# Optimization experiments

Measured on AMD Instinct MI355X. Metric: run time of the kernel, lower is better.

## Reference

```python
import jax, jax.numpy as jnp
import numpy as np

N = 50000
E = 600000
D_IN, D_HID, D_OUT = 128, 128, 64


def gcn_conv(x, edge_index, W, b):
    """PyG GCNConv: add self-loops, symmetric deg^{-1/2} normalization,
    linear transform, scatter-add aggregation, bias."""
    n = x.shape[0]
    loop = jnp.arange(n, dtype=edge_index.dtype)
    src = jnp.concatenate([edge_index[0], loop])
    dst = jnp.concatenate([edge_index[1], loop])
    h = x @ W  # [N, out]
    deg = jax.ops.segment_sum(jnp.ones_like(dst, dtype=h.dtype), dst, num_segments=n)
    dinv = jnp.where(deg > 0, jax.lax.rsqrt(jnp.maximum(deg, 1e-12)), 0.0)
    norm = dinv[src] * dinv[dst]  # [E+N]
    msg = h[src] * norm[:, None]  # gather + scale
    out = jax.ops.segment_sum(msg, dst, num_segments=n)  # scatter-add
    return out + b


def setup_inputs() -> dict:
    key = jax.random.key(0)
    k1, k2, k3, k4 = jax.random.split(key, 4)
    x = jax.random.normal(k1, (N, D_IN), dtype=jnp.float32)
    edge_index = jax.random.randint(k2, (2, E), 0, N, dtype=jnp.int64)
    s1 = (1.0 / np.sqrt(D_IN)).astype(np.float32) if False else np.float32(1.0 / np.sqrt(D_IN))
    s2 = np.float32(1.0 / np.sqrt(D_HID))
    W1 = jax.random.normal(k3, (D_IN, D_HID), dtype=jnp.float32) * s1
    b1 = jnp.zeros((D_HID,), dtype=jnp.float32)
    W2 = jax.random.normal(k4, (D_HID, D_OUT), dtype=jnp.float32) * s2
    b2 = jnp.zeros((D_OUT,), dtype=jnp.float32)
    return {"x": x, "edge_index": edge_index, "W1": W1, "b1": b1, "W2": W2, "b2": b2}


def reference(x, edge_index, W1, b1, W2, b2):
    # eval mode: dropout p = 0
    h = jax.nn.relu(gcn_conv(x, edge_index, W1, b1))
    return gcn_conv(h, edge_index, W2, b2)
```

## Files before the change

kernel.cpp:

```cpp
#include <hip/hip_runtime.h>
#include <hip/hip_bf16.h>
#include <stdint.h>

#define DIN 128
#define DHID 128
#define DOUT2 64

__device__ __forceinline__ unsigned short f2bf(float f) {
    unsigned u = __float_as_uint(f);
    u += 0x7fffu + ((u >> 16) & 1u);
    return (unsigned short)(u >> 16);
}
__device__ __forceinline__ float bf2f(unsigned short b) {
    return __uint_as_float(((unsigned)b) << 16);
}
__device__ __forceinline__ float bflo(unsigned v) { return __uint_as_float(v << 16); }
__device__ __forceinline__ float bfhi(unsigned v) { return __uint_as_float(v & 0xffff0000u); }

__global__ void detect_i64_kernel(const unsigned* ei, int* flag) {
    int t = threadIdx.x;
    unsigned hi = ei[2 * t + 1];
    unsigned long long vote = __ballot(hi == 0u);
    if (t == 0) *flag = (vote == ~0ull) ? 1 : 0;
}

__global__ void deg_count_kernel(const int* ei32, const long long* ei64, const int* flag,
                                 unsigned* deg, int E) {
    int e = blockIdx.x * blockDim.x + threadIdx.x;
    if (e >= E) return;
    int mode = *flag;
    int d = mode ? (int)ei64[(size_t)E + e] : ei32[(size_t)E + e];
    atomicAdd(&deg[d], 1u);
}

__global__ void dinv_kernel(const unsigned* deg, float* dinv, int N) {
    int i = blockIdx.x * blockDim.x + threadIdx.x;
    if (i < N) dinv[i] = 1.0f / sqrtf((float)(deg[i] + 1u));
}

__global__ __launch_bounds__(256) void scan_blocksum_kernel(const unsigned* deg, int* bsum,
                                                            int N) {
    __shared__ int s[256];
    int t = threadIdx.x;
    int base = blockIdx.x * 1024 + t * 4;
    int sum = 0;
    if (base + 3 < N) {
        int4 v = *(const int4*)((const int*)deg + base);
        sum = v.x + v.y + v.z + v.w;
    } else {
        for (int j = 0; j < 4; j++)
            if (base + j < N) sum += (int)deg[base + j];
    }
    s[t] = sum;
    __syncthreads();
    for (int off = 128; off > 0; off >>= 1) {
        if (t < off) s[t] += s[t + off];
        __syncthreads();
    }
    if (t == 0) bsum[blockIdx.x] = s[0];
}

__global__ __launch_bounds__(256) void scan_bsum_kernel(int* bsum, int* row_ptr, int nb, int N) {
    __shared__ int s[256];
    int t = threadIdx.x;
    int v = (t < nb) ? bsum[t] : 0;
    s[t] = v;
    __syncthreads();
    for (int off = 1; off < 256; off <<= 1) {
        int u = (t >= off) ? s[t - off] : 0;
        __syncthreads();
        s[t] += u;
        __syncthreads();
    }
    if (t < nb) bsum[t] = s[t] - v;
    if (t == 255) row_ptr[N] = s[255];
}

__global__ __launch_bounds__(256) void scan_write_kernel(const unsigned* deg, const int* bsum,
                                                         int* row_ptr, int* cursor, int N) {
    __shared__ int s[256];
    int t = threadIdx.x;
    int base = blockIdx.x * 1024 + t * 4;
    int d[4];
    int sum = 0;
#pragma unroll
    for (int j = 0; j < 4; j++) {
        int idx = base + j;
        d[j] = (idx < N) ? (int)deg[idx] : 0;
        sum += d[j];
    }
    s[t] = sum;
    __syncthreads();
    for (int off = 1; off < 256; off <<= 1) {
        int u = (t >= off) ? s[t - off] : 0;
        __syncthreads();
        s[t] += u;
        __syncthreads();
    }
    int run = bsum[blockIdx.x] + s[t] - sum;
#pragma unroll
    for (int j = 0; j < 4; j++) {
        int idx = base + j;
        if (idx < N) {
            row_ptr[idx] = run;
            cursor[idx] = run;
            run += d[j];
        }
    }
}

__global__ void scatter_kernel(const int* ei32, const long long* ei64, const int* flag,
                               const float* dinv, int* cursor, int* csr_src, float* csr_w,
                               int E) {
    int e = blockIdx.x * blockDim.x + threadIdx.x;
    if (e >= E) return;
    int mode = *flag;
    int s, d;
    if (mode) {
        s = (int)ei64[e];
        d = (int)ei64[(size_t)E + e];
    } else {
        s = ei32[e];
        d = ei32[(size_t)E + e];
    }
    int pos = atomicAdd(&cursor[d], 1);
    csr_src[pos] = s;
    csr_w[pos] = dinv[s];
}

template <int DO, typename AT>
__global__ __launch_bounds__(256, 2) void gemm_kernel(const AT* __restrict__ A,
                                                      const float* __restrict__ W,
                                                      unsigned short* __restrict__ out, int M) {
    constexpr int CG  = DO / 4;
    constexpr int TYN = 256 / CG;
    constexpr int RM  = 64 / TYN;
    __shared__ float As[64 * 64];
    __shared__ float Bs[64 * DO];
    const int tid = threadIdx.x;
    const int row0 = blockIdx.x * 64;
    const int tx = tid % CG, ty = tid / CG;

    float acc[RM][4];
#pragma unroll
    for (int r = 0; r < RM; r++) acc[r][0] = acc[r][1] = acc[r][2] = acc[r][3] = 0.f;

    for (int k0 = 0; k0 < 128; k0 += 64) {
        for (int idx = tid; idx < 64 * 16; idx += 256) {
            int r = idx >> 4, cc = idx & 15;
            int row = row0 + r;
            float4 v = make_float4(0.f, 0.f, 0.f, 0.f);
            if (row < M) {
                if constexpr (sizeof(AT) == 4) {
                    v = ((const float4*)A)[(size_t)row * 32 + (k0 >> 2) + cc];
                } else {
                    ushort4 u = ((const ushort4*)A)[(size_t)row * 32 + (k0 >> 2) + cc];
                    v = make_float4(bf2f(u.x), bf2f(u.y), bf2f(u.z), bf2f(u.w));
                }
            }
            ((float4*)As)[idx] = v;
        }
        for (int idx = tid; idx < 64 * CG; idx += 256) {
            int r = idx / CG, cc = idx % CG;
            ((float4*)Bs)[idx] = ((const float4*)W)[(size_t)(k0 + r) * CG + cc];
        }
        __syncthreads();
#pragma unroll 8
        for (int k = 0; k < 64; k++) {
            float4 b = ((const float4*)Bs)[k * CG + tx];
#pragma unroll
            for (int r = 0; r < RM; r++) {
                float a = As[(ty * RM + r) * 64 + k];
                acc[r][0] = fmaf(a, b.x, acc[r][0]);
                acc[r][1] = fmaf(a, b.y, acc[r][1]);
                acc[r][2] = fmaf(a, b.z, acc[r][2]);
                acc[r][3] = fmaf(a, b.w, acc[r][3]);
            }
        }
        __syncthreads();
    }
#pragma unroll
    for (int r = 0; r < RM; r++) {
        int row = row0 + ty * RM + r;
        if (row < M) {
            ushort4 v;
            v.x = f2bf(acc[r][0]);
            v.y = f2bf(acc[r][1]);
            v.z = f2bf(acc[r][2]);
            v.w = f2bf(acc[r][3]);
            ((ushort4*)out)[(size_t)row * CG + tx] = v;
        }
    }
}

template <int D, bool RELU, typename OT>
__global__ __launch_bounds__(256) void agg_kernel(const unsigned short* __restrict__ h,
                                                  const int* __restrict__ csr_src,
                                                  const float* __restrict__ csr_w,
                                                  const int* __restrict__ row_ptr,
                                                  const float* __restrict__ dinv,
                                                  const float* __restrict__ bias,
                                                  OT* __restrict__ out, int N) {
    const int wid = threadIdx.x >> 6;
    const int lane = threadIdx.x & 63;
    const int i = blockIdx.x * 4 + wid;
    if (i >= N) return;
    const float di = dinv[i];
    const int start = row_ptr[i], end = row_ptr[i + 1];

    if constexpr (D == 128) {
        const unsigned* hu = (const unsigned*)h;
        unsigned sv = hu[(size_t)i * 64 + lane];
        float a0 = di * bflo(sv), b0 = di * bfhi(sv);
        float a1 = 0.f, b1 = 0.f;
        int j = start;
        for (; j + 4 <= end; j += 4) {
            int s0 = csr_src[j], s1 = csr_src[j + 1], s2 = csr_src[j + 2], s3 = csr_src[j + 3];
            float w0 = csr_w[j], w1 = csr_w[j + 1], w2 = csr_w[j + 2], w3 = csr_w[j + 3];
            unsigned v0 = hu[(size_t)s0 * 64 + lane];
            unsigned v1 = hu[(size_t)s1 * 64 + lane];
            unsigned v2 = hu[(size_t)s2 * 64 + lane];
            unsigned v3 = hu[(size_t)s3 * 64 + lane];
            a0 = fmaf(w0, bflo(v0), a0);
            b0 = fmaf(w0, bfhi(v0), b0);
            a1 = fmaf(w1, bflo(v1), a1);
            b1 = fmaf(w1, bfhi(v1), b1);
            a0 = fmaf(w2, bflo(v2), a0);
            b0 = fmaf(w2, bfhi(v2), b0);
            a1 = fmaf(w3, bflo(v3), a1);
            b1 = fmaf(w3, bfhi(v3), b1);
        }
        for (; j < end; ++j) {
            int s0 = csr_src[j];
            float w0 = csr_w[j];
            unsigned v0 = hu[(size_t)s0 * 64 + lane];
            a0 = fmaf(w0, bflo(v0), a0);
            b0 = fmaf(w0, bfhi(v0), b0);
        }
        float rx = di * (a0 + a1) + bias[2 * lane];
        float ry = di * (b0 + b1) + bias[2 * lane + 1];
        if (RELU) {
            rx = fmaxf(rx, 0.f);
            ry = fmaxf(ry, 0.f);
        }
        if constexpr (sizeof(OT) == 2) {
            unsigned pv = (unsigned)f2bf(rx) | ((unsigned)f2bf(ry) << 16);
            ((unsigned*)out)[(size_t)i * 64 + lane] = pv;
        } else {
            float2 pv = make_float2(rx, ry);
            ((float2*)out)[(size_t)i * 64 + lane] = pv;
        }
    } else {
        float a0 = di * bf2f(h[(size_t)i * 64 + lane]);
        float a1 = 0.f;
        int j = start;
        for (; j + 4 <= end; j += 4) {
            int s0 = csr_src[j], s1 = csr_src[j + 1], s2 = csr_src[j + 2], s3 = csr_src[j + 3];
            float w0 = csr_w[j], w1 = csr_w[j + 1], w2 = csr_w[j + 2], w3 = csr_w[j + 3];
            float v0 = bf2f(h[(size_t)s0 * 64 + lane]);
            float v1 = bf2f(h[(size_t)s1 * 64 + lane]);
            float v2 = bf2f(h[(size_t)s2 * 64 + lane]);
            float v3 = bf2f(h[(size_t)s3 * 64 + lane]);
            a0 = fmaf(w0, v0, a0);
            a1 = fmaf(w1, v1, a1);
            a0 = fmaf(w2, v2, a0);
            a1 = fmaf(w3, v3, a1);
        }
        for (; j < end; ++j) {
            a0 = fmaf(csr_w[j], bf2f(h[(size_t)csr_src[j] * 64 + lane]), a0);
        }
        float r = di * (a0 + a1) + bias[lane];
        if (RELU) r = fmaxf(r, 0.f);
        if constexpr (sizeof(OT) == 2) {
            out[(size_t)i * 64 + lane] = (OT)f2bf(r);
        } else {
            out[(size_t)i * 64 + lane] = r;
        }
    }
}

extern "C" void kernel_launch(void* const* d_in, const int* in_sizes, int n_in,
                              void* d_out, int out_size, void* d_ws, size_t ws_size,
                              hipStream_t stream) {
    const float* x  = (const float*)d_in[0];
    const void*  ei = d_in[1];
    const float* W1 = (const float*)d_in[2];
    const float* b1 = (const float*)d_in[3];
    const float* W2 = (const float*)d_in[4];
    const float* b2 = (const float*)d_in[5];
    float* out = (float*)d_out;

    const int N = in_sizes[0] / DIN;
    const int E = in_sizes[1] / 2;

    char* ws = (char*)d_ws;
    size_t off = 0;
    auto alloc = [&](size_t bytes) -> void* {
        void* p = ws + off;
        off += (bytes + 255) & ~(size_t)255;
        return p;
    };
    unsigned*       deg  = (unsigned*)alloc((size_t)N * 4);
    float*          dinv = (float*)alloc((size_t)N * 4);
    int*            rowp = (int*)alloc((size_t)(N + 1) * 4);
    int*            curs = (int*)alloc((size_t)N * 4);
    int*            flag = (int*)alloc(256);
    int*            bsum = (int*)alloc(1024 * 4);
    int*            csrs = (int*)alloc((size_t)E * 4);
    float*          csrw = (float*)alloc((size_t)E * 4);
    unsigned short* h1   = (unsigned short*)alloc((size_t)N * DHID * 2);
    unsigned short* o1   = (unsigned short*)alloc((size_t)N * DHID * 2);
    unsigned short* h2   = h1;

    const int nb = (N + 1023) / 1024;

    hipMemsetAsync(deg, 0, (size_t)N * 4, stream);
    detect_i64_kernel<<<1, 64, 0, stream>>>((const unsigned*)ei, flag);
    deg_count_kernel<<<(E + 255) / 256, 256, 0, stream>>>((const int*)ei, (const long long*)ei,
                                                          flag, deg, E);
    dinv_kernel<<<(N + 255) / 256, 256, 0, stream>>>(deg, dinv, N);
    scan_blocksum_kernel<<<nb, 256, 0, stream>>>(deg, bsum, N);
    scan_bsum_kernel<<<1, 256, 0, stream>>>(bsum, rowp, nb, N);
    scan_write_kernel<<<nb, 256, 0, stream>>>(deg, bsum, rowp, curs, N);
    scatter_kernel<<<(E + 255) / 256, 256, 0, stream>>>((const int*)ei, (const long long*)ei,
                                                        flag, dinv, curs, csrs, csrw, E);
    gemm_kernel<DHID, float><<<(N + 63) / 64, 256, 0, stream>>>(x, W1, h1, N);
    agg_kernel<DHID, true, unsigned short><<<(N + 3) / 4, 256, 0, stream>>>(h1, csrs, csrw, rowp,
                                                                            dinv, b1, o1, N);
    gemm_kernel<DOUT2, unsigned short><<<(N + 63) / 64, 256, 0, stream>>>(o1, W2, h2, N);
    agg_kernel<DOUT2, false, float><<<(N + 3) / 4, 256, 0, stream>>>(h2, csrs, csrw, rowp, dinv,
                                                                     b2, out, N);
}
```

Baseline: 274.6 us.

## Fuse degree count with first GEMM, fold dinv into scan, pack CSR entries

Runs the layer-1 GEMM and the degree-count atomics in one launch so the independent work can overlap, and computes dinv inside the block-sum scan kernel, which removes two launches. When N fits in 16 bits, each CSR entry is packed into a single 32-bit word holding the source index and an fp16 copy of its dinv weight. This halves CSR traffic in both aggregation passes. The cost is fp16 rounding of the edge weights and a second code path for large graphs.

```diff
diff --git a/kernel.cpp b/kernel.cpp
--- a/kernel.cpp
+++ b/kernel.cpp
@@ -1,5 +1,5 @@
 #include <hip/hip_runtime.h>
-#include <hip/hip_bf16.h>
+#include <hip/hip_fp16.h>
 #include <stdint.h>
 
 #define DIN 128
@@ -16,6 +16,12 @@
 }
 __device__ __forceinline__ float bflo(unsigned v) { return __uint_as_float(v << 16); }
 __device__ __forceinline__ float bfhi(unsigned v) { return __uint_as_float(v & 0xffff0000u); }
+__device__ __forceinline__ unsigned short f2h(float f) {
+    return __half_as_ushort(__float2half_rn(f));
+}
+__device__ __forceinline__ float h2f(unsigned bits) {
+    return __half2float(__ushort_as_half((unsigned short)bits));
+}
 
 __global__ void detect_i64_kernel(const unsigned* ei, int* flag) {
     int t = threadIdx.x;
@@ -24,121 +30,15 @@
     if (t == 0) *flag = (vote == ~0ull) ? 1 : 0;
 }
 
-__global__ void deg_count_kernel(const int* ei32, const long long* ei64, const int* flag,
-                                 unsigned* deg, int E) {
-    int e = blockIdx.x * blockDim.x + threadIdx.x;
-    if (e >= E) return;
-    int mode = *flag;
-    int d = mode ? (int)ei64[(size_t)E + e] : ei32[(size_t)E + e];
-    atomicAdd(&deg[d], 1u);
-}
-
-__global__ void dinv_kernel(const unsigned* deg, float* dinv, int N) {
-    int i = blockIdx.x * blockDim.x + threadIdx.x;
-    if (i < N) dinv[i] = 1.0f / sqrtf((float)(deg[i] + 1u));
-}
-
-__global__ __launch_bounds__(256) void scan_blocksum_kernel(const unsigned* deg, int* bsum,
-                                                            int N) {
-    __shared__ int s[256];
-    int t = threadIdx.x;
-    int base = blockIdx.x * 1024 + t * 4;
-    int sum = 0;
-    if (base + 3 < N) {
-        int4 v = *(const int4*)((const int*)deg + base);
-        sum = v.x + v.y + v.z + v.w;
-    } else {
-        for (int j = 0; j < 4; j++)
-            if (base + j < N) sum += (int)deg[base + j];
-    }
-    s[t] = sum;
-    __syncthreads();
-    for (int off = 128; off > 0; off >>= 1) {
-        if (t < off) s[t] += s[t + off];
-        __syncthreads();
-    }
-    if (t == 0) bsum[blockIdx.x] = s[0];
-}
-
-__global__ __launch_bounds__(256) void scan_bsum_kernel(int* bsum, int* row_ptr, int nb, int N) {
-    __shared__ int s[256];
-    int t = threadIdx.x;
-    int v = (t < nb) ? bsum[t] : 0;
-    s[t] = v;
-    __syncthreads();
-    for (int off = 1; off < 256; off <<= 1) {
-        int u = (t >= off) ? s[t - off] : 0;
-        __syncthreads();
-        s[t] += u;
-        __syncthreads();
-    }
-    if (t < nb) bsum[t] = s[t] - v;
-    if (t == 255) row_ptr[N] = s[255];
-}
-
-__global__ __launch_bounds__(256) void scan_write_kernel(const unsigned* deg, const int* bsum,
-                                                         int* row_ptr, int* cursor, int N) {
-    __shared__ int s[256];
-    int t = threadIdx.x;
-    int base = blockIdx.x * 1024 + t * 4;
-    int d[4];
-    int sum = 0;
-#pragma unroll
-    for (int j = 0; j < 4; j++) {
-        int idx = base + j;
-        d[j] = (idx < N) ? (int)deg[idx] : 0;
-        sum += d[j];
-    }
-    s[t] = sum;
-    __syncthreads();
-    for (int off = 1; off < 256; off <<= 1) {
-        int u = (t >= off) ? s[t - off] : 0;
-        __syncthreads();
-        s[t] += u;
-        __syncthreads();
-    }
-    int run = bsum[blockIdx.x] + s[t] - sum;
-#pragma unroll
-    for (int j = 0; j < 4; j++) {
-        int idx = base + j;
-        if (idx < N) {
-            row_ptr[idx] = run;
-            cursor[idx] = run;
-            run += d[j];
-        }
-    }
-}
-
-__global__ void scatter_kernel(const int* ei32, const long long* ei64, const int* flag,
-                               const float* dinv, int* cursor, int* csr_src, float* csr_w,
-                               int E) {
-    int e = blockIdx.x * blockDim.x + threadIdx.x;
-    if (e >= E) return;
-    int mode = *flag;
-    int s, d;
-    if (mode) {
-        s = (int)ei64[e];
-        d = (int)ei64[(size_t)E + e];
-    } else {
-        s = ei32[e];
-        d = ei32[(size_t)E + e];
-    }
-    int pos = atomicAdd(&cursor[d], 1);
-    csr_src[pos] = s;
-    csr_w[pos] = dinv[s];
-}
-
 template <int DO, typename AT>
-__global__ __launch_bounds__(256, 2) void gemm_kernel(const AT* __restrict__ A,
-                                                      const float* __restrict__ W,
-                                                      unsigned short* __restrict__ out, int M) {
+__device__ __forceinline__ void gemm_block(const AT* __restrict__ A, const float* __restrict__ W,
+                                           unsigned short* __restrict__ out, int M, int bx,
+                                           float* As, float* Bs) {
     constexpr int CG  = DO / 4;
     constexpr int TYN = 256 / CG;
     constexpr int RM  = 64 / TYN;
-    __shared__ float As[64 * 64];
-    __shared__ float Bs[64 * DO];
     const int tid = threadIdx.x;
-    const int row0 = blockIdx.x * 64;
+    const int row0 = bx * 64;
     const int tx = tid % CG, ty = tid / CG;
 
     float acc[RM][4];
@@ -193,10 +93,162 @@
     }
 }
 
-template <int D, bool RELU, typename OT>
+__global__ __launch_bounds__(256, 2) void fused_gemm_deg_kernel(
+    const float* __restrict__ A, const float* __restrict__ W, unsigned short* __restrict__ out,
+    int M, int gemmBlocks, const int* ei32, const long long* ei64, const int* flag,
+    unsigned* deg, int E) {
+    __shared__ float As[64 * 64];
+    __shared__ float Bs[64 * DHID];
+    if ((int)blockIdx.x < gemmBlocks) {
+        gemm_block<DHID, float>(A, W, out, M, blockIdx.x, As, Bs);
+    } else {
+        int e = (blockIdx.x - gemmBlocks) * 256 + threadIdx.x;
+        if (e < E) {
+            int mode = *flag;
+            int d = mode ? (int)ei64[(size_t)E + e] : ei32[(size_t)E + e];
+            atomicAdd(&deg[d], 1u);
+        }
+    }
+}
+
+template <int DO, typename AT>
+__global__ __launch_bounds__(256, 2) void gemm_kernel(const AT* __restrict__ A,
+                                                      const float* __restrict__ W,
+                                                      unsigned short* __restrict__ out, int M) {
+    __shared__ float As[64 * 64];
+    __shared__ float Bs[64 * DO];
+    gemm_block<DO, AT>(A, W, out, M, blockIdx.x, As, Bs);
+}
+
+__global__ __launch_bounds__(256) void scan_blocksum_kernel(const unsigned* deg, int* bsum,
+                                                            float* dinv, int N) {
+    __shared__ int s[256];
+    int t = threadIdx.x;
+    int base = blockIdx.x * 1024 + t * 4;
+    int sum = 0;
+    if (base + 3 < N) {
+        int4 v = *(const int4*)((const int*)deg + base);
+        sum = v.x + v.y + v.z + v.w;
+        float4 dv;
+        dv.x = rsqrtf((float)(v.x + 1));
+        dv.y = rsqrtf((float)(v.y + 1));
+        dv.z = rsqrtf((float)(v.z + 1));
+        dv.w = rsqrtf((float)(v.w + 1));
+        *(float4*)(dinv + base) = dv;
+    } else {
+        for (int j = 0; j < 4; j++)
+            if (base + j < N) {
+                int d = (int)deg[base + j];
+                sum += d;
+                dinv[base + j] = rsqrtf((float)(d + 1));
+            }
+    }
+    s[t] = sum;
+    __syncthreads();
+    for (int off = 128; off > 0; off >>= 1) {
+        if (t < off) s[t] += s[t + off];
+        __syncthreads();
+    }
+    if (t == 0) bsum[blockIdx.x] = s[0];
+}
+
+__global__ __launch_bounds__(256) void scan_bsum_kernel(int* bsum, int* row_ptr, int nb, int N) {
+    __shared__ int s[256];
+    int t = threadIdx.x;
+    int v = (t < nb) ? bsum[t] : 0;
+    s[t] = v;
+    __syncthreads();
+    for (int off = 1; off < 256; off <<= 1) {
+        int u = (t >= off) ? s[t - off] : 0;
+        __syncthreads();
+        s[t] += u;
+        __syncthreads();
+    }
+    if (t < nb) bsum[t] = s[t] - v;
+    if (t == 255) row_ptr[N] = s[255];
+}
+
+__global__ __launch_bounds__(256) void scan_write_kernel(const unsigned* deg, const int* bsum,
+                                                         int* row_ptr, int* cursor, int N) {
+    __shared__ int s[256];
+    int t = threadIdx.x;
+    int base = blockIdx.x * 1024 + t * 4;
+    int d[4];
+    int sum = 0;
+#pragma unroll
+    for (int j = 0; j < 4; j++) {
+        int idx = base + j;
+        d[j] = (idx < N) ? (int)deg[idx] : 0;
+        sum += d[j];
+    }
+    s[t] = sum;
+    __syncthreads();
+    for (int off = 1; off < 256; off <<= 1) {
+        int u = (t >= off) ? s[t - off] : 0;
+        __syncthreads();
+        s[t] += u;
+        __syncthreads();
+    }
+    int run = bsum[blockIdx.x] + s[t] - sum;
+#pragma unroll
+    for (int j = 0; j < 4; j++) {
+        int idx = base + j;
+        if (idx < N) {
+            row_ptr[idx] = run;
+            cursor[idx] = run;
+            run += d[j];
+        }
+    }
+}
+
+__global__ void scatter_pack32_kernel(const int* ei32, const long long* ei64, const int* flag,
+                                      const float* dinv, int* cursor, unsigned* csr, int E) {
+    int e = blockIdx.x * blockDim.x + threadIdx.x;
+    if (e >= E) return;
+    int mode = *flag;
+    int s, d;
+    if (mode) {
+        s = (int)ei64[e];
+        d = (int)ei64[(size_t)E + e];
+    } else {
+        s = ei32[e];
+        d = ei32[(size_t)E + e];
+    }
+    int pos = atomicAdd(&cursor[d], 1);
+    csr[pos] = (unsigned)s | ((unsigned)f2h(dinv[s]) << 16);
+}
+
+__global__ void scatter_pack64_kernel(const int* ei32, const long long* ei64, const int* flag,
+                                      const float* dinv, int* cursor, unsigned long long* csr,
+                                      int E) {
+    int e = blockIdx.x * blockDim.x + threadIdx.x;
+    if (e >= E) return;
+    int mode = *flag;
+    int s, d;
+    if (mode) {
+        s = (int)ei64[e];
+        d = (int)ei64[(size_t)E + e];
+    } else {
+        s = ei32[e];
+        d = ei32[(size_t)E + e];
+    }
+    int pos = atomicAdd(&cursor[d], 1);
+    csr[pos] = (unsigned long long)(unsigned)s |
+               ((unsigned long long)__float_as_uint(dinv[s]) << 32);
+}
+
+__device__ __forceinline__ void unpack(unsigned p, int& s, float& w) {
+    s = (int)(p & 0xffffu);
+    w = h2f(p >> 16);
+}
+__device__ __forceinline__ void unpack(unsigned long long p, int& s, float& w) {
+    s = (int)(unsigned)(p & 0xffffffffu);
+    w = __uint_as_float((unsigned)(p >> 32));
+}
+
+template <int D, bool RELU, typename OT, typename CT>
 __global__ __launch_bounds__(256) void agg_kernel(const unsigned short* __restrict__ h,
-                                                  const int* __restrict__ csr_src,
-                                                  const float* __restrict__ csr_w,
+                                                  const CT* __restrict__ csr,
                                                   const int* __restrict__ row_ptr,
                                                   const float* __restrict__ dinv,
                                                   const float* __restrict__ bias,
@@ -215,8 +267,13 @@
         float a1 = 0.f, b1 = 0.f;
         int j = start;
         for (; j + 4 <= end; j += 4) {
-            int s0 = csr_src[j], s1 = csr_src[j + 1], s2 = csr_src[j + 2], s3 = csr_src[j + 3];
-            float w0 = csr_w[j], w1 = csr_w[j + 1], w2 = csr_w[j + 2], w3 = csr_w[j + 3];
+            CT p0 = csr[j], p1 = csr[j + 1], p2 = csr[j + 2], p3 = csr[j + 3];
+            int s0, s1, s2, s3;
+            float w0, w1, w2, w3;
+            unpack(p0, s0, w0);
+            unpack(p1, s1, w1);
+            unpack(p2, s2, w2);
+            unpack(p3, s3, w3);
             unsigned v0 = hu[(size_t)s0 * 64 + lane];
             unsigned v1 = hu[(size_t)s1 * 64 + lane];
             unsigned v2 = hu[(size_t)s2 * 64 + lane];
@@ -231,14 +288,16 @@
             b1 = fmaf(w3, bfhi(v3), b1);
         }
         for (; j < end; ++j) {
-            int s0 = csr_src[j];
-            float w0 = csr_w[j];
+            int s0;
+            float w0;
+            unpack(csr[j], s0, w0);
             unsigned v0 = hu[(size_t)s0 * 64 + lane];
             a0 = fmaf(w0, bflo(v0), a0);
             b0 = fmaf(w0, bfhi(v0), b0);
         }
-        float rx = di * (a0 + a1) + bias[2 * lane];
-        float ry = di * (b0 + b1) + bias[2 * lane + 1];
+        float2 bv = ((const float2*)bias)[lane];
+        float rx = di * (a0 + a1) + bv.x;
+        float ry = di * (b0 + b1) + bv.y;
         if (RELU) {
             rx = fmaxf(rx, 0.f);
             ry = fmaxf(ry, 0.f);
@@ -247,16 +306,20 @@
             unsigned pv = (unsigned)f2bf(rx) | ((unsigned)f2bf(ry) << 16);
             ((unsigned*)out)[(size_t)i * 64 + lane] = pv;
         } else {
-            float2 pv = make_float2(rx, ry);
-            ((float2*)out)[(size_t)i * 64 + lane] = pv;
+            ((float2*)out)[(size_t)i * 64 + lane] = make_float2(rx, ry);
         }
     } else {
         float a0 = di * bf2f(h[(size_t)i * 64 + lane]);
         float a1 = 0.f;
         int j = start;
         for (; j + 4 <= end; j += 4) {
-            int s0 = csr_src[j], s1 = csr_src[j + 1], s2 = csr_src[j + 2], s3 = csr_src[j + 3];
-            float w0 = csr_w[j], w1 = csr_w[j + 1], w2 = csr_w[j + 2], w3 = csr_w[j + 3];
+            CT p0 = csr[j], p1 = csr[j + 1], p2 = csr[j + 2], p3 = csr[j + 3];
+            int s0, s1, s2, s3;
+            float w0, w1, w2, w3;
+            unpack(p0, s0, w0);
+            unpack(p1, s1, w1);
+            unpack(p2, s2, w2);
+            unpack(p3, s3, w3);
             float v0 = bf2f(h[(size_t)s0 * 64 + lane]);
             float v1 = bf2f(h[(size_t)s1 * 64 + lane]);
             float v2 = bf2f(h[(size_t)s2 * 64 + lane]);
@@ -267,7 +330,10 @@
             a1 = fmaf(w3, v3, a1);
         }
         for (; j < end; ++j) {
-            a0 = fmaf(csr_w[j], bf2f(h[(size_t)csr_src[j] * 64 + lane]), a0);
+            int s0;
+            float w0;
+            unpack(csr[j], s0, w0);
+            a0 = fmaf(w0, bf2f(h[(size_t)s0 * 64 + lane]), a0);
         }
         float r = di * (a0 + a1) + bias[lane];
         if (RELU) r = fmaxf(r, 0.f);
@@ -306,28 +372,41 @@
     int*            curs = (int*)alloc((size_t)N * 4);
     int*            flag = (int*)alloc(256);
     int*            bsum = (int*)alloc(1024 * 4);
-    int*            csrs = (int*)alloc((size_t)E * 4);
-    float*          csrw = (float*)alloc((size_t)E * 4);
+    void*           csr  = alloc((size_t)E * 8);
     unsigned short* h1   = (unsigned short*)alloc((size_t)N * DHID * 2);
     unsigned short* o1   = (unsigned short*)alloc((size_t)N * DHID * 2);
     unsigned short* h2   = h1;
 
     const int nb = (N + 1023) / 1024;
+    const int gemmBlocks = (N + 63) / 64;
+    const int degBlocks = (E + 255) / 256;
 
     hipMemsetAsync(deg, 0, (size_t)N * 4, stream);
     detect_i64_kernel<<<1, 64, 0, stream>>>((const unsigned*)ei, flag);
-    deg_count_kernel<<<(E + 255) / 256, 256, 0, stream>>>((const int*)ei, (const long long*)ei,
-                                                          flag, deg, E);
-    dinv_kernel<<<(N + 255) / 256, 256, 0, stream>>>(deg, dinv, N);
-    scan_blocksum_kernel<<<nb, 256, 0, stream>>>(deg, bsum, N);
+    fused_gemm_deg_kernel<<<gemmBlocks + degBlocks, 256, 0, stream>>>(
+        x, W1, h1, N, gemmBlocks, (const int*)ei, (const long long*)ei, flag, deg, E);
+    scan_blocksum_kernel<<<nb, 256, 0, stream>>>(deg, bsum, dinv, N);
     scan_bsum_kernel<<<1, 256, 0, stream>>>(bsum, rowp, nb, N);
     scan_write_kernel<<<nb, 256, 0, stream>>>(deg, bsum, rowp, curs, N);
-    scatter_kernel<<<(E + 255) / 256, 256, 0, stream>>>((const int*)ei, (const long long*)ei,
-                                                        flag, dinv, curs, csrs, csrw, E);
-    gemm_kernel<DHID, float><<<(N + 63) / 64, 256, 0, stream>>>(x, W1, h1, N);
-    agg_kernel<DHID, true, unsigned short><<<(N + 3) / 4, 256, 0, stream>>>(h1, csrs, csrw, rowp,
-                                                                            dinv, b1, o1, N);
-    gemm_kernel<DOUT2, unsigned short><<<(N + 63) / 64, 256, 0, stream>>>(o1, W2, h2, N);
-    agg_kernel<DOUT2, false, float><<<(N + 3) / 4, 256, 0, stream>>>(h2, csrs, csrw, rowp, dinv,
-                                                                     b2, out, N);
-}
+
+    if (N <= 65535) {
+        unsigned* csr32 = (unsigned*)csr;
+        scatter_pack32_kernel<<<degBlocks, 256, 0, stream>>>(
+            (const int*)ei, (const long long*)ei, flag, dinv, curs, csr32, E);
+        agg_kernel<DHID, true, unsigned short, unsigned><<<(N + 3) / 4, 256, 0, stream>>>(
+            h1, csr32, rowp, dinv, b1, o1, N);
+        gemm_kernel<DOUT2, unsigned short><<<gemmBlocks, 256, 0, stream>>>(o1, W2, h2, N);
+        agg_kernel<DOUT2, false, float, unsigned><<<(N + 3) / 4, 256, 0, stream>>>(
+            h2, csr32, rowp, dinv, b2, out, N);
+    } else {
+        unsigned long long* csr64 = (unsigned long long*)csr;
+        scatter_pack64_kernel<<<degBlocks, 256, 0, stream>>>(
+            (const int*)ei, (const long long*)ei, flag, dinv, curs, csr64, E);
+        agg_kernel<DHID, true, unsigned short, unsigned long long><<<(N + 3) / 4, 256, 0,
+                                                                     stream>>>(h1, csr64, rowp,
+                                                                               dinv, b1, o1, N);
+        gemm_kernel<DOUT2, unsigned short><<<gemmBlocks, 256, 0, stream>>>(o1, W2, h2, N);
+        agg_kernel<DOUT2, false, float, unsigned long long><<<(N + 3) / 4, 256, 0, stream>>>(
+            h2, csr64, rowp, dinv, b2, out, N);
+    }
+}
```

After: 243.2 us. 11.4% less time.
